# Performance work log

Measured on AMD Instinct MI355X. Metric: run time of the kernel, lower is better.

Reference implementation:

```python
import jax, jax.numpy as jnp
import numpy as np

HIDDEN = 1024
NUM_HEADS = 16
HEAD_DIM = HIDDEN // NUM_HEADS
EPS = 1e-05


def setup_inputs() -> dict:
    key = jax.random.key(0)
    ks = jax.random.split(key, 6)
    B, S = 4, 2048
    x = jax.random.normal(ks[0], (B, S, HIDDEN), dtype=jnp.float32)
    # trunc_normal_(std=0.02) approximated by scaled normal
    w_in = jax.random.normal(ks[1], (3 * HIDDEN, HIDDEN), dtype=jnp.float32) * 0.02
    b_in = jax.random.normal(ks[2], (3 * HIDDEN,), dtype=jnp.float32) * 0.02
    w_norm = jnp.ones((HIDDEN,), dtype=jnp.float32)
    lim = 1.0 / np.sqrt(HIDDEN)
    w_out = jax.random.uniform(ks[3], (HIDDEN, HIDDEN), dtype=jnp.float32, minval=-lim, maxval=lim)
    b_out = jax.random.uniform(ks[4], (HIDDEN,), dtype=jnp.float32, minval=-lim, maxval=lim)
    return {"x": x, "w_in": w_in, "b_in": b_in, "w_norm": w_norm, "w_out": w_out, "b_out": b_out}


def _rms_norm(x, w, eps):
    var = jnp.mean(jnp.square(x), axis=-1, keepdims=True)
    return x * jax.lax.rsqrt(var + eps) * w


def reference(x, w_in, b_in, w_norm, w_out, b_out):
    B, S, _ = x.shape
    xn = _rms_norm(x, w_norm, EPS)
    qkv = jnp.einsum('bsd,ed->bse', xn, w_in) + b_in  # [B,S,3*HIDDEN]
    q, k, v = jnp.split(qkv, 3, axis=-1)
    # [B,S,H*D] -> [B,H,S,D]
    def split_heads(t):
        return t.reshape(B, S, NUM_HEADS, HEAD_DIM).transpose(0, 2, 1, 3)
    q, k, v = split_heads(q), split_heads(k), split_heads(v)
    scale = 1.0 / np.sqrt(HEAD_DIM)
    scores = jnp.einsum('bhqd,bhkd->bhqk', q, k) * scale
    attn = jax.nn.softmax(scores, axis=-1)
    o = jnp.einsum('bhqk,bhkd->bhqd', attn, v)
    o = o.transpose(0, 2, 1, 3).reshape(B, S, HIDDEN)
    return jnp.einsum('bsd,ed->bse', o, w_out) + b_out
```

## Files before the change

### kernel.cpp

```cpp
#include <hip/hip_runtime.h>
#include <stdint.h>

typedef short bf16x4 __attribute__((ext_vector_type(4)));
typedef short bf16x8 __attribute__((ext_vector_type(8)));
typedef _Float16 f16x8 __attribute__((ext_vector_type(8)));
typedef float f32x4 __attribute__((ext_vector_type(4)));
typedef float f32x16 __attribute__((ext_vector_type(16)));
typedef unsigned int u32x4 __attribute__((ext_vector_type(4)));
typedef unsigned int u32x2 __attribute__((ext_vector_type(2)));

#if __has_builtin(__builtin_amdgcn_exp2f)
#define EXP2 __builtin_amdgcn_exp2f
#else
#define EXP2 exp2f
#endif

__device__ __forceinline__ short f2bf(float f) {
  union { float f; uint32_t u; } v; v.f = f;
  uint32_t r = (v.u + 0x7fffu + ((v.u >> 16) & 1u)) >> 16;
  return (short)(uint16_t)r;
}

__device__ __forceinline__ unsigned cvtpk_bf16(float lo, float hi) {
  unsigned r;
  asm("v_cvt_pk_bf16_f32 %0, %1, %2" : "=v"(r) : "v"(lo), "v"(hi));
  return r;
}

#if __has_builtin(__builtin_amdgcn_permlane32_swap)
__device__ __forceinline__ void plane32_swap(unsigned& a, unsigned& b) {
  u32x2 r = __builtin_amdgcn_permlane32_swap(a, b, false, false);
  a = r[0]; b = r[1];
}
__device__ __forceinline__ float xhalf_max(float x) {
  unsigned xu = __builtin_bit_cast(unsigned, x);
  u32x2 r = __builtin_amdgcn_permlane32_swap(xu, xu, false, false);
  return fmaxf(__builtin_bit_cast(float, r[0]), __builtin_bit_cast(float, r[1]));
}
__device__ __forceinline__ float xhalf_sum(float x) {
  unsigned xu = __builtin_bit_cast(unsigned, x);
  u32x2 r = __builtin_amdgcn_permlane32_swap(xu, xu, false, false);
  return __builtin_bit_cast(float, r[0]) + __builtin_bit_cast(float, r[1]);
}
#else
__device__ __forceinline__ void plane32_swap(unsigned& a, unsigned& b) {
  asm("s_nop 1\n\tv_permlane32_swap_b32 %0, %1" : "+v"(a), "+v"(b));
}
__device__ __forceinline__ float xhalf_max(float x) { return fmaxf(x, __shfl_xor(x, 32, 64)); }
__device__ __forceinline__ float xhalf_sum(float x) { return x + __shfl_xor(x, 32, 64); }
#endif

__device__ __forceinline__ float fmax3(float a, float b, float c) {
  return fmaxf(fmaxf(a, b), c);
}

__device__ __forceinline__ float tmax16(const f32x16& s) {
  float a0 = fmax3(s[0], s[1], s[2]);
  float a1 = fmax3(s[3], s[4], s[5]);
  float a2 = fmax3(s[6], s[7], s[8]);
  float a3 = fmax3(s[9], s[10], s[11]);
  float a4 = fmax3(s[12], s[13], s[14]);
  float b0 = fmax3(a0, a1, s[15]);
  float b1 = fmax3(a2, a3, a4);
  return fmaxf(b0, b1);
}
__device__ __forceinline__ float tsum16(const f32x16& s) {
  float a0 = (s[0] + s[1]) + (s[2] + s[3]);
  float a1 = (s[4] + s[5]) + (s[6] + s[7]);
  float a2 = (s[8] + s[9]) + (s[10] + s[11]);
  float a3 = (s[12] + s[13]) + (s[14] + s[15]);
  return (a0 + a1) + (a2 + a3);
}

__device__ __forceinline__ f32x16 zero16() {
  f32x16 z;
#pragma unroll
  for (int i = 0; i < 16; ++i) z[i] = 0.f;
  return z;
}

__device__ __forceinline__ void gld_lds16(const void* g, void* l) {
  __builtin_amdgcn_global_load_lds(
      (__attribute__((address_space(1))) const void*)g,
      (__attribute__((address_space(3))) void*)l, 16, 0, 0);
}

__global__ __launch_bounds__(256) void k_rmsnorm(const float* __restrict__ x,
                                                 const float* __restrict__ wn,
                                                 short* __restrict__ xn) {
  const int row = blockIdx.x;
  const int t = threadIdx.x;
  const float4 v = reinterpret_cast<const float4*>(x + (size_t)row * 1024)[t];
  float ss = v.x * v.x + v.y * v.y + v.z * v.z + v.w * v.w;
#pragma unroll
  for (int m = 32; m >= 1; m >>= 1) ss += __shfl_xor(ss, m, 64);
  __shared__ float red[4];
  if ((t & 63) == 0) red[t >> 6] = ss;
  __syncthreads();
  const float tot = red[0] + red[1] + red[2] + red[3];
  const float rr = rsqrtf(tot * (1.0f / 1024.0f) + 1e-5f);
  const float4 g = reinterpret_cast<const float4*>(wn)[t];
  bf16x4 o;
  o[0] = f2bf(v.x * rr * g.x);
  o[1] = f2bf(v.y * rr * g.y);
  o[2] = f2bf(v.z * rr * g.z);
  o[3] = f2bf(v.w * rr * g.w);
  reinterpret_cast<bf16x4*>(xn + (size_t)row * 1024)[t] = o;
}

__global__ __launch_bounds__(256) void k_cast_bf(const float* __restrict__ in,
                                                 short* __restrict__ out, int n4) {
  int i = blockIdx.x * 256 + threadIdx.x;
  if (i >= n4) return;
  float4 v = reinterpret_cast<const float4*>(in)[i];
  bf16x4 o;
  o[0] = f2bf(v.x); o[1] = f2bf(v.y); o[2] = f2bf(v.z); o[3] = f2bf(v.w);
  reinterpret_cast<bf16x4*>(out)[i] = o;
}

__global__ __launch_bounds__(256) void k_cast_f16(const float* __restrict__ in,
                                                  _Float16* __restrict__ out, int n4) {
  int i = blockIdx.x * 256 + threadIdx.x;
  if (i >= n4) return;
  float4 v = reinterpret_cast<const float4*>(in)[i];
  _Float16 o[4] = {(_Float16)v.x, (_Float16)v.y, (_Float16)v.z, (_Float16)v.w};
  reinterpret_cast<ulong1*>(out)[i] = *reinterpret_cast<ulong1*>(o);
}

__global__ __launch_bounds__(256) void k_gemm_qkv(const short* __restrict__ A,
                                                  const short* __restrict__ B,
                                                  const float* __restrict__ bias,
                                                  short* __restrict__ qb,
                                                  short* __restrict__ kb,
                                                  short* __restrict__ vb) {
  __shared__ __align__(16) short As[128 * 32];
  __shared__ __align__(16) short Bs[128 * 32];
  const int t = threadIdx.x;
  const int orig = blockIdx.y * 24 + blockIdx.x;
  const int swz = (orig & 7) * 192 + (orig >> 3);
  const long bn0 = (long)(swz % 24) * 128;
  const long bm0 = (long)(swz / 24) * 128;
  const int w = t >> 6, l = t & 63;
  const int wr = (w >> 1) * 64, wc = (w & 1) * 64;
  const int lm = l & 15, h = l >> 4;
  f32x4 acc[4][4];
#pragma unroll
  for (int i = 0; i < 4; ++i)
#pragma unroll
    for (int j = 0; j < 4; ++j) acc[i][j] = (f32x4){0.f, 0.f, 0.f, 0.f};
  const int srow = t >> 2, scol = (t & 3) * 8;
  const short* Ag = A + (bm0 + srow) * 1024 + scol;
  const short* Bg = B + (bn0 + srow) * 1024 + scol;
  short* AsP = As + t * 8;
  short* BsP = Bs + t * 8;
  for (int kt = 0; kt < 32; ++kt) {
    const int k0 = kt << 5;
    gld_lds16(Ag + k0, AsP);
    gld_lds16(Ag + k0 + 64 * 1024, AsP + 2048);
    gld_lds16(Bg + k0, BsP);
    gld_lds16(Bg + k0 + 64 * 1024, BsP + 2048);
    __syncthreads();
    bf16x8 af[4], bfr[4];
#pragma unroll
    for (int mi = 0; mi < 4; ++mi)
      af[mi] = *reinterpret_cast<const bf16x8*>(As + (wr + mi * 16 + lm) * 32 + h * 8);
#pragma unroll
    for (int ni = 0; ni < 4; ++ni)
      bfr[ni] = *reinterpret_cast<const bf16x8*>(Bs + (wc + ni * 16 + lm) * 32 + h * 8);
    __builtin_amdgcn_s_setprio(1);
#pragma unroll
    for (int mi = 0; mi < 4; ++mi)
#pragma unroll
      for (int ni = 0; ni < 4; ++ni)
        acc[mi][ni] = __builtin_amdgcn_mfma_f32_16x16x32_bf16(af[mi], bfr[ni], acc[mi][ni], 0, 0, 0);
    __builtin_amdgcn_s_setprio(0);
    __syncthreads();
  }
#pragma unroll
  for (int ni = 0; ni < 4; ++ni) {
    const int ncol = (int)bn0 + wc + ni * 16 + lm;
    const float bv = bias[ncol];
    const int which = ncol >> 10;
    const int e = ncol & 1023;
#pragma unroll
    for (int mi = 0; mi < 4; ++mi) {
#pragma unroll
      for (int r = 0; r < 4; ++r) {
        const long mrow = bm0 + wr + mi * 16 + h * 4 + r;
        const float val = acc[mi][ni][r] + bv;
        const long off = (((mrow >> 11) * 16 + (e >> 6)) * 2048 + (mrow & 2047)) * 64 + (e & 63);
        if (which == 0) qb[off] = f2bf(val * 0.18033688011112042f);
        else if (which == 1) kb[off] = f2bf(val);
        else vb[off] = f2bf(val);
      }
    }
  }
}

__global__ __launch_bounds__(256) void k_gemm_out(const _Float16* __restrict__ A,
                                                  const _Float16* __restrict__ B,
                                                  const float* __restrict__ bias,
                                                  float* __restrict__ outp) {
  __shared__ __align__(16) _Float16 As[128 * 32];
  __shared__ __align__(16) _Float16 Bs[128 * 32];
  const int t = threadIdx.x;
  const int orig = blockIdx.y * 8 + blockIdx.x;
  const int swz = (orig & 7) * 64 + (orig >> 3);
  const long bn0 = (long)(swz % 8) * 128;
  const long bm0 = (long)(swz / 8) * 128;
  const int w = t >> 6, l = t & 63;
  const int wr = (w >> 1) * 64, wc = (w & 1) * 64;
  const int lm = l & 15, h = l >> 4;
  f32x4 acc[4][4];
#pragma unroll
  for (int i = 0; i < 4; ++i)
#pragma unroll
    for (int j = 0; j < 4; ++j) acc[i][j] = (f32x4){0.f, 0.f, 0.f, 0.f};
  const int srow = t >> 2, scol = (t & 3) * 8;
  const _Float16* Ag = A + (bm0 + srow) * 1024 + scol;
  const _Float16* Bg = B + (bn0 + srow) * 1024 + scol;
  _Float16* AsP = As + t * 8;
  _Float16* BsP = Bs + t * 8;
  for (int kt = 0; kt < 32; ++kt) {
    const int k0 = kt << 5;
    gld_lds16(Ag + k0, AsP);
    gld_lds16(Ag + k0 + 64 * 1024, AsP + 2048);
    gld_lds16(Bg + k0, BsP);
    gld_lds16(Bg + k0 + 64 * 1024, BsP + 2048);
    __syncthreads();
    f16x8 af[4], bfr[4];
#pragma unroll
    for (int mi = 0; mi < 4; ++mi)
      af[mi] = *reinterpret_cast<const f16x8*>(As + (wr + mi * 16 + lm) * 32 + h * 8);
#pragma unroll
    for (int ni = 0; ni < 4; ++ni)
      bfr[ni] = *reinterpret_cast<const f16x8*>(Bs + (wc + ni * 16 + lm) * 32 + h * 8);
    __builtin_amdgcn_s_setprio(1);
#pragma unroll
    for (int mi = 0; mi < 4; ++mi)
#pragma unroll
      for (int ni = 0; ni < 4; ++ni)
        acc[mi][ni] = __builtin_amdgcn_mfma_f32_16x16x32_f16(af[mi], bfr[ni], acc[mi][ni], 0, 0, 0);
    __builtin_amdgcn_s_setprio(0);
    __syncthreads();
  }
#pragma unroll
  for (int ni = 0; ni < 4; ++ni) {
    const int ncol = (int)bn0 + wc + ni * 16 + lm;
    const float bv = bias[ncol];
#pragma unroll
    for (int mi = 0; mi < 4; ++mi) {
#pragma unroll
      for (int r = 0; r < 4; ++r) {
        const long mrow = bm0 + wr + mi * 16 + h * 4 + r;
        outp[mrow * 1024 + ncol] = acc[mi][ni][r] + bv;
      }
    }
  }
}

__global__ __launch_bounds__(256) void k_transpose_v(const short* __restrict__ v,
                                                     short* __restrict__ vt) {
  __shared__ short tile[64][72];
  const int bh = blockIdx.y, st = blockIdx.x;
  const int t = threadIdx.x;
  const int r = t >> 2, c0 = (t & 3) * 16;
  const short* src = v + ((size_t)(bh * 2048 + st * 64 + r)) * 64 + c0;
  bf16x8 a = *reinterpret_cast<const bf16x8*>(src);
  bf16x8 b = *reinterpret_cast<const bf16x8*>(src + 8);
#pragma unroll
  for (int j = 0; j < 8; ++j) tile[r][c0 + j] = a[j];
#pragma unroll
  for (int j = 0; j < 8; ++j) tile[r][c0 + 8 + j] = b[j];
  __syncthreads();
  __align__(16) short tmp[16];
#pragma unroll
  for (int j = 0; j < 16; ++j) tmp[j] = tile[c0 + j][r];
  short* dst = vt + ((size_t)(bh * 64 + r)) * 2048 + st * 64 + c0;
  *reinterpret_cast<bf16x8*>(dst) = *reinterpret_cast<const bf16x8*>(tmp);
  *reinterpret_cast<bf16x8*>(dst + 8) = *reinterpret_cast<const bf16x8*>(tmp + 8);
}

__global__ __launch_bounds__(256, 2) void k_attn(const short* __restrict__ q,
                                                 const short* __restrict__ k,
                                                 const short* __restrict__ vt,
                                                 _Float16* __restrict__ o) {
  __shared__ __align__(16) short lds[4][8192];
  const int orig = blockIdx.y * 8 + blockIdx.x;
  const int work = (orig & 7) * 64 + (orig >> 3);
  const int bh = work >> 3;
  const int qt = work & 7;
  const int t = threadIdx.x;
  const int w = t >> 6, l = t & 63;
  const int lq = l & 31, hh = l >> 5;
  const int xr = lq & 7;
  const int qbase = qt * 256 + w * 64;
  short* Kb = &lds[w][0];
  short* Vb = &lds[w][4096];

  bf16x8 qf[2][4];
#pragma unroll
  for (int qh = 0; qh < 2; ++qh) {
    const short* qp = q + ((size_t)(bh * 2048 + qbase + qh * 32 + lq)) * 64 + hh * 8;
#pragma unroll
    for (int db = 0; db < 4; ++db)
      qf[qh][db] = *reinterpret_cast<const bf16x8*>(qp + db * 16);
  }

  const short* kh = k + (size_t)bh * 2048 * 64;
  const short* vh = vt + (size_t)bh * 64 * 2048;
  const short* ks4[4];
  const short* vs4[4];
#pragma unroll
  for (int i = 0; i < 4; ++i) {
    const int g = i * 64 + l;
    const int uK = g ^ ((g >> 3) & 7);
    ks4[i] = kh + uK * 8;
    const int vr = g >> 2;
    const int vc = (g & 3) ^ (vr & 3);
    vs4[i] = vh + vr * 2048 + vc * 8;
  }

  int koff[4], voff[2][2];
#pragma unroll
  for (int db = 0; db < 4; ++db)
    koff[db] = (lq * 8 + ((db * 2 + hh) ^ xr)) * 8;
#pragma unroll
  for (int dt = 0; dt < 2; ++dt)
#pragma unroll
    for (int kg = 0; kg < 2; ++kg)
      voff[dt][kg] = ((dt * 32 + lq) * 4 + ((kg * 2 + hh) ^ (lq & 3))) * 8;

  f32x16 oa00 = zero16(), oa01 = zero16();
  f32x16 oa10 = zero16(), oa11 = zero16();
  float mr0 = -1e30f, mr1 = -1e30f, lr0 = 0.f, lr1 = 0.f;

#pragma unroll
  for (int p = 0; p < 2; ++p) {
#pragma unroll
    for (int i = 0; i < 4; ++i)
      gld_lds16(ks4[i] + p * 2048, Kb + p * 2048 + i * 512 + l * 8);
#pragma unroll
    for (int i = 0; i < 4; ++i)
      gld_lds16(vs4[i] + p * 32, Vb + p * 2048 + i * 512 + l * 8);
  }

#pragma unroll 2
  for (int kt = 0; kt < 64; ++kt) {
    asm volatile("s_waitcnt vmcnt(8)" ::: "memory");
    const int buf = kt & 1;
    const short* kb_ = Kb + buf * 2048;
    const short* vb_ = Vb + buf * 2048;
    bf16x8 kf[4], vfr[2][2];
#pragma unroll
    for (int db = 0; db < 4; ++db)
      kf[db] = *reinterpret_cast<const bf16x8*>(kb_ + koff[db]);
#pragma unroll
    for (int dt = 0; dt < 2; ++dt)
#pragma unroll
      for (int kg = 0; kg < 2; ++kg)
        vfr[dt][kg] = *reinterpret_cast<const bf16x8*>(vb_ + voff[dt][kg]);
    asm volatile("s_waitcnt lgkmcnt(0)" ::: "memory");
    __builtin_amdgcn_sched_barrier(0);
    int kn = kt + 2; if (kn > 63) kn = 63;
#pragma unroll
    for (int i = 0; i < 4; ++i)
      gld_lds16(ks4[i] + kn * 2048, (short*)kb_ + i * 512 + l * 8);
#pragma unroll
    for (int i = 0; i < 4; ++i)
      gld_lds16(vs4[i] + kn * 32, (short*)vb_ + i * 512 + l * 8);

    f32x16 s0 = zero16(), s1 = zero16();
    __builtin_amdgcn_s_setprio(1);
#pragma unroll
    for (int db = 0; db < 4; ++db) {
      s0 = __builtin_amdgcn_mfma_f32_32x32x16_bf16(kf[db], qf[0][db], s0, 0, 0, 0);
      s1 = __builtin_amdgcn_mfma_f32_32x32x16_bf16(kf[db], qf[1][db], s1, 0, 0, 0);
    }
    __builtin_amdgcn_s_setprio(0);
    float tm0 = xhalf_max(tmax16(s0));
    float tm1 = xhalf_max(tmax16(s1));
    if (!__all((tm0 <= mr0 + 8.f) && (tm1 <= mr1 + 8.f))) {
      const float mn0 = fmaxf(mr0, tm0), mn1 = fmaxf(mr1, tm1);
      const float c0 = EXP2(mr0 - mn0), c1 = EXP2(mr1 - mn1);
      lr0 *= c0; lr1 *= c1;
#pragma unroll
      for (int r = 0; r < 16; ++r) {
        oa00[r] *= c0; oa01[r] *= c0;
        oa10[r] *= c1; oa11[r] *= c1;
      }
      mr0 = mn0; mr1 = mn1;
    }
#pragma unroll
    for (int r = 0; r < 16; ++r) {
      s0[r] = EXP2(s0[r] - mr0);
      s1[r] = EXP2(s1[r] - mr1);
    }
    lr0 += tsum16(s0);
    lr1 += tsum16(s1);
    __builtin_amdgcn_s_setprio(1);
#pragma unroll
    for (int kg = 0; kg < 2; ++kg) {
      const int b0 = kg * 8;
      unsigned p00 = cvtpk_bf16(s0[b0 + 0], s0[b0 + 1]);
      unsigned p01 = cvtpk_bf16(s0[b0 + 2], s0[b0 + 3]);
      unsigned p02 = cvtpk_bf16(s0[b0 + 4], s0[b0 + 5]);
      unsigned p03 = cvtpk_bf16(s0[b0 + 6], s0[b0 + 7]);
      plane32_swap(p00, p02);
      plane32_swap(p01, p03);
      u32x4 pw0 = {p00, p01, p02, p03};
      bf16x8 pf0 = *reinterpret_cast<bf16x8*>(&pw0);
      unsigned p10 = cvtpk_bf16(s1[b0 + 0], s1[b0 + 1]);
      unsigned p11 = cvtpk_bf16(s1[b0 + 2], s1[b0 + 3]);
      unsigned p12 = cvtpk_bf16(s1[b0 + 4], s1[b0 + 5]);
      unsigned p13 = cvtpk_bf16(s1[b0 + 6], s1[b0 + 7]);
      plane32_swap(p10, p12);
      plane32_swap(p11, p13);
      u32x4 pw1 = {p10, p11, p12, p13};
      bf16x8 pf1 = *reinterpret_cast<bf16x8*>(&pw1);
      oa00 = __builtin_amdgcn_mfma_f32_32x32x16_bf16(vfr[0][kg], pf0, oa00, 0, 0, 0);
      oa10 = __builtin_amdgcn_mfma_f32_32x32x16_bf16(vfr[0][kg], pf1, oa10, 0, 0, 0);
      oa01 = __builtin_amdgcn_mfma_f32_32x32x16_bf16(vfr[1][kg], pf0, oa01, 0, 0, 0);
      oa11 = __builtin_amdgcn_mfma_f32_32x32x16_bf16(vfr[1][kg], pf1, oa11, 0, 0, 0);
    }
    __builtin_amdgcn_s_setprio(0);
  }
  const float inv0 = 1.0f / xhalf_sum(lr0);
  const float inv1 = 1.0f / xhalf_sum(lr1);
  const int b = bh >> 4, hd = bh & 15;
  _Float16* ob0 = o + ((size_t)(b * 2048 + qbase + lq)) * 1024 + hd * 64;
  _Float16* ob1 = ob0 + 32 * 1024;
#pragma unroll
  for (int r2 = 0; r2 < 16; ++r2) {
    const int d0 = (r2 & 3) + 8 * (r2 >> 2) + 4 * hh;
    ob0[d0] = (_Float16)(oa00[r2] * inv0);
    ob0[d0 + 32] = (_Float16)(oa01[r2] * inv0);
    ob1[d0] = (_Float16)(oa10[r2] * inv1);
    ob1[d0 + 32] = (_Float16)(oa11[r2] * inv1);
  }
}

extern "C" void kernel_launch(void* const* d_in, const int* in_sizes, int n_in,
                              void* d_out, int out_size, void* d_ws, size_t ws_size,
                              hipStream_t stream) {
  const float* x = (const float*)d_in[0];
  const float* w_in = (const float*)d_in[1];
  const float* b_in = (const float*)d_in[2];
  const float* w_norm = (const float*)d_in[3];
  const float* w_out = (const float*)d_in[4];
  const float* b_out = (const float*)d_in[5];
  float* out = (float*)d_out;
  char* ws = (char*)d_ws;
  short* xn = (short*)(ws);
  short* win_b = (short*)(ws + 16777216);
  _Float16* wout_h = (_Float16*)(ws + 23068672);
  short* qb = (short*)(ws + 25165824);
  short* kb = (short*)(ws + 41943040);
  short* vb = (short*)(ws + 58720256);
  short* vt = (short*)(ws + 75497472);
  _Float16* ob = (_Float16*)vb;

  k_cast_bf<<<3072, 256, 0, stream>>>(w_in, win_b, 786432);
  k_cast_f16<<<1024, 256, 0, stream>>>(w_out, wout_h, 262144);
  k_rmsnorm<<<8192, 256, 0, stream>>>(x, w_norm, xn);
  k_gemm_qkv<<<dim3(24, 64), 256, 0, stream>>>(xn, win_b, b_in, qb, kb, vb);
  k_transpose_v<<<dim3(32, 64), 256, 0, stream>>>(vb, vt);
  k_attn<<<dim3(8, 64), 256, 0, stream>>>(qb, kb, vt, ob);
  k_gemm_out<<<dim3(8, 64), 256, 0, stream>>>(ob, wout_h, b_out, out);
}
```

Before: 226.6 us.

## Share K/V LDS tiles across waves in 128-thread attention blocks

Each attention block now has two waves, each owning 64 query rows, instead of four waves that each staged their own private K/V copy. The two waves load one shared double-buffered K/V tile cooperatively, so each wave issues half the global-to-LDS copies and the block uses a quarter of the LDS. The grid doubles to 1024 blocks, allowing more resident blocks per CU. In exchange, two workgroup barriers are added per key tile to keep the shared buffers consistent.

```diff
diff --git a/kernel.cpp b/kernel.cpp
--- a/kernel.cpp
+++ b/kernel.cpp
@@ -281,22 +281,20 @@
   *reinterpret_cast<bf16x8*>(dst + 8) = *reinterpret_cast<const bf16x8*>(tmp + 8);
 }
 
-__global__ __launch_bounds__(256, 2) void k_attn(const short* __restrict__ q,
+__global__ __launch_bounds__(128, 4) void k_attn(const short* __restrict__ q,
                                                  const short* __restrict__ k,
                                                  const short* __restrict__ vt,
                                                  _Float16* __restrict__ o) {
-  __shared__ __align__(16) short lds[4][8192];
-  const int orig = blockIdx.y * 8 + blockIdx.x;
-  const int work = (orig & 7) * 64 + (orig >> 3);
-  const int bh = work >> 3;
-  const int qt = work & 7;
+  __shared__ __align__(16) short S[8192];
+  const int orig = blockIdx.y * 16 + blockIdx.x;
+  const int work = (orig & 7) * 128 + (orig >> 3);
+  const int bh = work >> 4;
+  const int qt = work & 15;
   const int t = threadIdx.x;
   const int w = t >> 6, l = t & 63;
   const int lq = l & 31, hh = l >> 5;
   const int xr = lq & 7;
-  const int qbase = qt * 256 + w * 64;
-  short* Kb = &lds[w][0];
-  short* Vb = &lds[w][4096];
+  const int qbase = qt * 128 + w * 64;
 
   bf16x8 qf[2][4];
 #pragma unroll
@@ -309,17 +307,17 @@
 
   const short* kh = k + (size_t)bh * 2048 * 64;
   const short* vh = vt + (size_t)bh * 64 * 2048;
-  const short* ks4[4];
-  const short* vs4[4];
-#pragma unroll
-  for (int i = 0; i < 4; ++i) {
-    const int g = i * 64 + l;
-    const int uK = g ^ ((g >> 3) & 7);
-    ks4[i] = kh + uK * 8;
-    const int vr = g >> 2;
-    const int vc = (g & 3) ^ (vr & 3);
-    vs4[i] = vh + vr * 2048 + vc * 8;
-  }
+  const short* ksA; const short* ksB; const short* vsA; const short* vsB;
+  {
+    const int gA = w * 64 + l, gB = 128 + w * 64 + l;
+    const int uA = gA ^ ((gA >> 3) & 7), uB = gB ^ ((gB >> 3) & 7);
+    ksA = kh + uA * 8;
+    ksB = kh + uB * 8;
+    vsA = vh + (gA >> 2) * 2048 + ((gA & 3) ^ ((gA >> 2) & 3)) * 8;
+    vsB = vh + (gB >> 2) * 2048 + ((gB & 3) ^ ((gB >> 2) & 3)) * 8;
+  }
+  const int gdA = (w * 64) * 8 + l * 8;
+  const int gdB = (128 + w * 64) * 8 + l * 8;
 
   int koff[4], voff[2][2];
 #pragma unroll
@@ -337,20 +335,21 @@
 
 #pragma unroll
   for (int p = 0; p < 2; ++p) {
-#pragma unroll
-    for (int i = 0; i < 4; ++i)
-      gld_lds16(ks4[i] + p * 2048, Kb + p * 2048 + i * 512 + l * 8);
-#pragma unroll
-    for (int i = 0; i < 4; ++i)
-      gld_lds16(vs4[i] + p * 32, Vb + p * 2048 + i * 512 + l * 8);
+    short* kb0 = S + p * 4096;
+    short* vb0 = S + p * 4096 + 2048;
+    gld_lds16(ksA + p * 2048, kb0 + gdA);
+    gld_lds16(ksB + p * 2048, kb0 + gdB);
+    gld_lds16(vsA + p * 32, vb0 + gdA);
+    gld_lds16(vsB + p * 32, vb0 + gdB);
   }
 
 #pragma unroll 2
   for (int kt = 0; kt < 64; ++kt) {
-    asm volatile("s_waitcnt vmcnt(8)" ::: "memory");
+    asm volatile("s_waitcnt vmcnt(4)" ::: "memory");
+    __builtin_amdgcn_s_barrier();
     const int buf = kt & 1;
-    const short* kb_ = Kb + buf * 2048;
-    const short* vb_ = Vb + buf * 2048;
+    short* kb_ = S + buf * 4096;
+    short* vb_ = S + buf * 4096 + 2048;
     bf16x8 kf[4], vfr[2][2];
 #pragma unroll
     for (int db = 0; db < 4; ++db)
@@ -362,13 +361,12 @@
         vfr[dt][kg] = *reinterpret_cast<const bf16x8*>(vb_ + voff[dt][kg]);
     asm volatile("s_waitcnt lgkmcnt(0)" ::: "memory");
     __builtin_amdgcn_sched_barrier(0);
+    __builtin_amdgcn_s_barrier();
     int kn = kt + 2; if (kn > 63) kn = 63;
-#pragma unroll
-    for (int i = 0; i < 4; ++i)
-      gld_lds16(ks4[i] + kn * 2048, (short*)kb_ + i * 512 + l * 8);
-#pragma unroll
-    for (int i = 0; i < 4; ++i)
-      gld_lds16(vs4[i] + kn * 32, (short*)vb_ + i * 512 + l * 8);
+    gld_lds16(ksA + kn * 2048, kb_ + gdA);
+    gld_lds16(ksB + kn * 2048, kb_ + gdB);
+    gld_lds16(vsA + kn * 32, vb_ + gdA);
+    gld_lds16(vsB + kn * 32, vb_ + gdB);
 
     f32x16 s0 = zero16(), s1 = zero16();
     __builtin_amdgcn_s_setprio(1);
@@ -465,6 +463,6 @@
   k_rmsnorm<<<8192, 256, 0, stream>>>(x, w_norm, xn);
   k_gemm_qkv<<<dim3(24, 64), 256, 0, stream>>>(xn, win_b, b_in, qb, kb, vb);
   k_transpose_v<<<dim3(32, 64), 256, 0, stream>>>(vb, vt);
-  k_attn<<<dim3(8, 64), 256, 0, stream>>>(qb, kb, vt, ob);
+  k_attn<<<dim3(16, 64), 128, 0, stream>>>(qb, kb, vt, ob);
   k_gemm_out<<<dim3(8, 64), 256, 0, stream>>>(ob, wout_h, b_out, out);
 }
```

After: 552.8 us. +144.0%, slower.
